# Kernel tuning notes

Measured on AMD Instinct MI355X. Metric: run time of the kernel, lower is better.

## Reference

```python
import jax, jax.numpy as jnp
import numpy as np


def setup_inputs() -> dict:
    key = jax.random.key(0)
    ks = jax.random.split(key, 6)
    B, N, D_in, D, Dg, H = 32, 256, 512, 256, 256, 512
    s = lambda f_in: 1.0 / np.sqrt(f_in)
    return {
        "xi": jax.random.normal(ks[0], (B, N, D_in), dtype=jnp.float32),
        "W_img": jax.random.normal(ks[1], (D_in, D), dtype=jnp.float32) * s(D_in),
        "b_img": jnp.zeros((D,), jnp.float32),
        "W_gnn_self": jax.random.normal(ks[2], (D, Dg), dtype=jnp.float32) * s(D),
        "W_gnn_nbr": jax.random.normal(ks[3], (D, Dg), dtype=jnp.float32) * s(D),
        "b_gnn": jnp.zeros((Dg,), jnp.float32),
        "W1": jax.random.normal(ks[4], (N * Dg, H), dtype=jnp.float32) * s(N * Dg),
        "b1": jnp.zeros((H,), jnp.float32),
        "W2": jax.random.normal(ks[5], (H, 1), dtype=jnp.float32) * s(H),
        "b2": jnp.zeros((1,), jnp.float32),
        "k": 10,
    }


def _knn_edges(xie, k):
    # xie: [B, N, D]. Per-image squared euclidean cdist + top-k (exclude self).
    B, N, _ = xie.shape
    x2 = jnp.sum(xie * xie, axis=-1)  # [B, N]
    d2 = x2[:, :, None] + x2[:, None, :] - 2.0 * jnp.einsum("bnd,bmd->bnm", xie, xie)
    big = jnp.asarray(1e30, d2.dtype)
    d2 = d2 + big * jnp.eye(N, dtype=d2.dtype)  # exclude self
    _, nbr = jax.lax.top_k(-d2, k)  # [B, N, k] neighbor (source) indices
    tgt = jnp.broadcast_to(jnp.arange(N)[None, :, None], (B, N, k))
    return nbr, tgt


def reference(xi, W_img, b_img, W_gnn_self, W_gnn_nbr, b_gnn, W1, b1, W2, b2, k):
    B, N, _ = xi.shape
    # image encoder -> per-node embeddings [B, N, D]
    xie = xi @ W_img + b_img
    # KNN graph build per image, then shift indices into one batched graph
    nbr, tgt = _knn_edges(xie, k)
    shift = (jnp.arange(B) * N)[:, None, None]
    src = (nbr + shift).reshape(-1)  # [B*N*k]
    dst = (tgt + shift).reshape(-1)  # [B*N*k]
    # batched graph conv: mean neighbor aggregation + self transform
    x_flat = xie.reshape(B * N, -1)
    agg = jax.ops.segment_sum(x_flat[src], dst, num_segments=B * N) / k
    gep = jax.nn.relu(x_flat @ W_gnn_self + agg @ W_gnn_nbr + b_gnn)
    gep = gep.reshape(B, N, -1)  # split_batch_graph
    # estimation MLP on flattened graph embedding
    h = jax.nn.relu(gep.reshape(B, -1) @ W1 + b1)
    out = h @ W2 + b2  # [B, 1]
    return xie, gep, out
```

## Files before the change

### kernel.cpp

```cpp
#include <hip/hip_runtime.h>

#define BB 32
#define NN 256
#define DIN 512
#define DD 256
#define HH 512
#define MM 8192
#define KSTR 16

typedef __attribute__((ext_vector_type(8))) __bf16 bf16x8;
typedef __attribute__((ext_vector_type(4))) float f32x4;
typedef unsigned short ushort_t;

typedef const float __attribute__((address_space(1)))* gas1f;
typedef const unsigned int __attribute__((address_space(1)))* gas1u;
typedef unsigned int __attribute__((address_space(3)))* las3u;

__device__ __forceinline__ unsigned short f2bf(float x) {
  unsigned u = __float_as_uint(x);
  u += 0x7FFFu + ((u >> 16) & 1u);
  return (unsigned short)(u >> 16);
}

__global__ __launch_bounds__(512) void k_enc(const float* __restrict__ A,
                                             const float* __restrict__ W,
                                             const float* __restrict__ bias,
                                             float* __restrict__ C,
                                             ushort_t* __restrict__ A_bf,
                                             float* __restrict__ xieT) {
  __shared__ float Asm[32][520];
  const int tid = threadIdx.x;
  const int mb0 = blockIdx.x * 32;
  const int cg = tid & 31;
  const int mh = (tid >> 5) & 7;
  const int team = tid >> 8;
#pragma unroll
  for (int i = 0; i < 8; ++i) {
    int idx = tid + i * 512;
    int m = idx >> 7;
    int kq = idx & 127;
    float4 v = *reinterpret_cast<const float4*>(&A[(size_t)(mb0 + m) * DIN + kq * 4]);
    *reinterpret_cast<float4*>(&Asm[m][kq * 4]) = v;
  }
  __syncthreads();
  float4 acc[4][2] = {};
  const int kt0 = team * 256;
  const float* wp = &W[(size_t)kt0 * DD + cg * 8];
  float4 wA[4][2], wB[4][2];
#pragma unroll
  for (int j = 0; j < 4; ++j) {
    wA[j][0] = *reinterpret_cast<const float4*>(&wp[(size_t)j * DD]);
    wA[j][1] = *reinterpret_cast<const float4*>(&wp[(size_t)j * DD + 4]);
  }
  for (int it = 0; it < 64; ++it) {
    if (it < 63) {
#pragma unroll
      for (int j = 0; j < 4; ++j) {
        wB[j][0] = *reinterpret_cast<const float4*>(&wp[(size_t)((it + 1) * 4 + j) * DD]);
        wB[j][1] = *reinterpret_cast<const float4*>(&wp[(size_t)((it + 1) * 4 + j) * DD + 4]);
      }
    }
    const int kk = kt0 + it * 4;
#pragma unroll
    for (int r = 0; r < 4; ++r) {
      float4 a = *reinterpret_cast<const float4*>(&Asm[mh * 4 + r][kk]);
#pragma unroll
      for (int h = 0; h < 2; ++h) {
        acc[r][h].x += a.x * wA[0][h].x; acc[r][h].y += a.x * wA[0][h].y;
        acc[r][h].z += a.x * wA[0][h].z; acc[r][h].w += a.x * wA[0][h].w;
        acc[r][h].x += a.y * wA[1][h].x; acc[r][h].y += a.y * wA[1][h].y;
        acc[r][h].z += a.y * wA[1][h].z; acc[r][h].w += a.y * wA[1][h].w;
        acc[r][h].x += a.z * wA[2][h].x; acc[r][h].y += a.z * wA[2][h].y;
        acc[r][h].z += a.z * wA[2][h].z; acc[r][h].w += a.z * wA[2][h].w;
        acc[r][h].x += a.w * wA[3][h].x; acc[r][h].y += a.w * wA[3][h].y;
        acc[r][h].z += a.w * wA[3][h].z; acc[r][h].w += a.w * wA[3][h].w;
      }
    }
#pragma unroll
    for (int j = 0; j < 4; ++j) {
      wA[j][0] = wB[j][0]; wA[j][1] = wB[j][1];
    }
  }
  __syncthreads();
  float* red = &Asm[0][0];
  if (team == 1) {
#pragma unroll
    for (int r = 0; r < 4; ++r) {
      *reinterpret_cast<float4*>(&red[(mh * 4 + r) * 256 + cg * 8]) = acc[r][0];
      *reinterpret_cast<float4*>(&red[(mh * 4 + r) * 256 + cg * 8 + 4]) = acc[r][1];
    }
  }
  __syncthreads();
  if (team == 0) {
    float4 bv0 = *reinterpret_cast<const float4*>(&bias[cg * 8]);
    float4 bv1 = *reinterpret_cast<const float4*>(&bias[cg * 8 + 4]);
#pragma unroll
    for (int r = 0; r < 4; ++r) {
      const int row = mb0 + mh * 4 + r;
      float4 o0 = *reinterpret_cast<float4*>(&red[(mh * 4 + r) * 256 + cg * 8]);
      float4 o1 = *reinterpret_cast<float4*>(&red[(mh * 4 + r) * 256 + cg * 8 + 4]);
      float4 s0, s1;
      s0.x = acc[r][0].x + o0.x + bv0.x; s0.y = acc[r][0].y + o0.y + bv0.y;
      s0.z = acc[r][0].z + o0.z + bv0.z; s0.w = acc[r][0].w + o0.w + bv0.w;
      s1.x = acc[r][1].x + o1.x + bv1.x; s1.y = acc[r][1].y + o1.y + bv1.y;
      s1.z = acc[r][1].z + o1.z + bv1.z; s1.w = acc[r][1].w + o1.w + bv1.w;
      *reinterpret_cast<float4*>(&C[(size_t)row * DD + cg * 8]) = s0;
      *reinterpret_cast<float4*>(&C[(size_t)row * DD + cg * 8 + 4]) = s1;
      ushort4 ob0, ob1;
      ob0.x = f2bf(s0.x); ob0.y = f2bf(s0.y); ob0.z = f2bf(s0.z); ob0.w = f2bf(s0.w);
      ob1.x = f2bf(s1.x); ob1.y = f2bf(s1.y); ob1.z = f2bf(s1.z); ob1.w = f2bf(s1.w);
      *reinterpret_cast<ushort4*>(&A_bf[(size_t)row * 512 + cg * 8]) = ob0;
      *reinterpret_cast<ushort4*>(&A_bf[(size_t)row * 512 + cg * 8 + 4]) = ob1;
      *reinterpret_cast<float4*>(&red[(mh * 4 + r) * 256 + cg * 8]) = s0;
      *reinterpret_cast<float4*>(&red[(mh * 4 + r) * 256 + cg * 8 + 4]) = s1;
    }
  }
  __syncthreads();
  {
    const int b = mb0 >> 8;
    const int n0b = mb0 & 255;
    const int d = tid >> 1;
    const int nh = (tid & 1) * 16;
    float tmp[16];
#pragma unroll
    for (int i = 0; i < 16; ++i) tmp[i] = red[(nh + i) * 256 + d];
    float* dst = &xieT[((size_t)b * 256 + d) * 256 + n0b + nh];
#pragma unroll
    for (int i = 0; i < 4; ++i)
      *reinterpret_cast<float4*>(&dst[i * 4]) = *reinterpret_cast<float4*>(&tmp[i * 4]);
  }
}

__global__ __launch_bounds__(256) void k_norm(const float* __restrict__ X,
                                              float* __restrict__ x2) {
  const int tid = threadIdx.x;
  const int row = blockIdx.x * 4 + (tid >> 6);
  const int lane = tid & 63;
  float4 v = *reinterpret_cast<const float4*>(&X[(size_t)row * DD + lane * 4]);
  float s = v.x * v.x + v.y * v.y + v.z * v.z + v.w * v.w;
#pragma unroll
  for (int off = 1; off < 64; off <<= 1) s += __shfl_xor(s, off);
  if (lane == 0) x2[row] = s;
}

__global__ __launch_bounds__(512) void k_dist(const float* __restrict__ xie,
                                              const float* __restrict__ xieT,
                                              const float* __restrict__ x2g,
                                              float* __restrict__ d2) {
  __shared__ float Asm[32][260];
  const int tid = threadIdx.x;
  const int b = blockIdx.x >> 3;
  const int n0b = (blockIdx.x & 7) * 32;
  const int base = b * 256;
  const int cg = tid & 31;
  const int rg = tid >> 5;
#pragma unroll
  for (int i = 0; i < 4; ++i) {
    int idx = tid + i * 512;
    int m = idx >> 6;
    int kq = idx & 63;
    float4 v = *reinterpret_cast<const float4*>(
        &xie[(size_t)(base + n0b + m) * DD + kq * 4]);
    *reinterpret_cast<float4*>(&Asm[m][kq * 4]) = v;
  }
  __syncthreads();
  float4 acc[2][2] = {};
  const float* wp = &xieT[(size_t)base * 256 + cg * 8];
  float4 wA[4][2], wB[4][2];
#pragma unroll
  for (int j = 0; j < 4; ++j) {
    wA[j][0] = *reinterpret_cast<const float4*>(&wp[(size_t)j * 256]);
    wA[j][1] = *reinterpret_cast<const float4*>(&wp[(size_t)j * 256 + 4]);
  }
  for (int it = 0; it < 64; ++it) {
    if (it < 63) {
#pragma unroll
      for (int j = 0; j < 4; ++j) {
        wB[j][0] = *reinterpret_cast<const float4*>(&wp[(size_t)((it + 1) * 4 + j) * 256]);
        wB[j][1] = *reinterpret_cast<const float4*>(&wp[(size_t)((it + 1) * 4 + j) * 256 + 4]);
      }
    }
#pragma unroll
    for (int r = 0; r < 2; ++r) {
      float4 a = *reinterpret_cast<const float4*>(&Asm[rg * 2 + r][it * 4]);
#pragma unroll
      for (int h = 0; h < 2; ++h) {
        acc[r][h].x += a.x * wA[0][h].x; acc[r][h].y += a.x * wA[0][h].y;
        acc[r][h].z += a.x * wA[0][h].z; acc[r][h].w += a.x * wA[0][h].w;
        acc[r][h].x += a.y * wA[1][h].x; acc[r][h].y += a.y * wA[1][h].y;
        acc[r][h].z += a.y * wA[1][h].z; acc[r][h].w += a.y * wA[1][h].w;
        acc[r][h].x += a.z * wA[2][h].x; acc[r][h].y += a.z * wA[2][h].y;
        acc[r][h].z += a.z * wA[2][h].z; acc[r][h].w += a.z * wA[2][h].w;
        acc[r][h].x += a.w * wA[3][h].x; acc[r][h].y += a.w * wA[3][h].y;
        acc[r][h].z += a.w * wA[3][h].z; acc[r][h].w += a.w * wA[3][h].w;
      }
    }
#pragma unroll
    for (int j = 0; j < 4; ++j) {
      wA[j][0] = wB[j][0]; wA[j][1] = wB[j][1];
    }
  }
#pragma unroll
  for (int r = 0; r < 2; ++r) {
    const int nl = n0b + rg * 2 + r;
    const float xn = x2g[base + nl];
#pragma unroll
    for (int h = 0; h < 2; ++h) {
      const float* accp = reinterpret_cast<const float*>(&acc[r][h]);
      float4 v;
      float* vv = reinterpret_cast<float*>(&v);
#pragma unroll
      for (int j2 = 0; j2 < 4; ++j2) {
        const int mc = cg * 8 + h * 4 + j2;
        float dv = xn + x2g[base + mc] - 2.0f * accp[j2];
        if (nl == mc) dv = 1e30f;
        vv[j2] = dv;
      }
      *reinterpret_cast<float4*>(&d2[(size_t)(base + nl) * 256 + cg * 8 + h * 4]) = v;
    }
  }
}

__global__ __launch_bounds__(256) void k_topkagg(const float* __restrict__ X,
                                                 const float* __restrict__ d2,
                                                 const int* __restrict__ kp,
                                                 ushort_t* __restrict__ A_bf) {
  __shared__ int nbrL[4][KSTR];
  const int tid = threadIdx.x;
  const int rw = tid >> 6;
  const int i = blockIdx.x * 4 + rw;
  const int lane = tid & 63;
  const int kcnt = kp[0];
  const float* row = d2 + (size_t)i * NN;
  float v0 = row[lane];
  float v1 = row[lane + 64];
  float v2 = row[lane + 128];
  float v3 = row[lane + 192];
  for (int it = 0; it < kcnt; ++it) {
    float v = v0; int idx = lane;
    if (v1 < v) { v = v1; idx = lane + 64; }
    if (v2 < v) { v = v2; idx = lane + 128; }
    if (v3 < v) { v = v3; idx = lane + 192; }
#pragma unroll
    for (int off = 1; off < 64; off <<= 1) {
      float ov = __shfl_xor(v, off);
      int oi = __shfl_xor(idx, off);
      if (ov < v || (ov == v && oi < idx)) { v = ov; idx = oi; }
    }
    if (lane == 0) nbrL[rw][it] = idx;
    const int slot = idx >> 6;
    if (lane == (idx & 63)) {
      if (slot == 0) v0 = 3e38f;
      else if (slot == 1) v1 = 3e38f;
      else if (slot == 2) v2 = 3e38f;
      else v3 = 3e38f;
    }
  }
  __syncthreads();
  {
    const int b = i >> 8;
    float4 s = make_float4(0.f, 0.f, 0.f, 0.f);
    for (int j = 0; j < kcnt; ++j) {
      const int nb = nbrL[rw][j];
      float4 v = *reinterpret_cast<const float4*>(
          &X[(size_t)(b * NN + nb) * DD + lane * 4]);
      s.x += v.x; s.y += v.y; s.z += v.z; s.w += v.w;
    }
    const float sc = 1.0f / (float)kcnt;
    ushort4 ob;
    ob.x = f2bf(s.x * sc); ob.y = f2bf(s.y * sc);
    ob.z = f2bf(s.z * sc); ob.w = f2bf(s.w * sc);
    *reinterpret_cast<ushort4*>(&A_bf[(size_t)i * 512 + 256 + lane * 4]) = ob;
  }
}

__global__ __launch_bounds__(256) void k_cvtw(const float* __restrict__ Ws,
                                              const float* __restrict__ Wn,
                                              ushort_t* __restrict__ B_bfT) {
  const int id = blockIdx.x * 256 + threadIdx.x;
  const int k = id >> 8;
  const int n = id & 255;
  float v = (k < 256) ? Ws[(size_t)k * 256 + n] : Wn[(size_t)(k - 256) * 256 + n];
  B_bfT[(size_t)n * 512 + k] = f2bf(v);
}

__global__ __launch_bounds__(256) void k_gnn(const ushort_t* __restrict__ A_bf,
                                             const ushort_t* __restrict__ B_bfT,
                                             const float* __restrict__ bias,
                                             float* __restrict__ C,
                                             ushort_t* __restrict__ gep_bf) {
  __shared__ ushort_t As[128 * 64];
  __shared__ ushort_t Bs[64 * 64];
  const int tid = threadIdx.x;
  const int m0 = blockIdx.x * 128, n0 = blockIdx.y * 64;
  const int l = tid & 63, w = tid >> 6;
  const int mw = (w & 1) * 64, nw = (w >> 1) * 32;
  f32x4 acc[4][2] = {};
  for (int kt = 0; kt < 8; ++kt) {
    const int kb = kt * 64;
    const int grow = w * 8 + (l >> 3);
    const int gcol = (l & 7) * 8;
#pragma unroll
    for (int it2 = 0; it2 < 4; ++it2) {
      __builtin_amdgcn_global_load_lds(
          (gas1u)&A_bf[(size_t)(m0 + it2 * 32 + grow) * 512 + kb + gcol],
          (las3u)((char*)As + it2 * 4096 + w * 1024), 16, 0, 0);
    }
#pragma unroll
    for (int it2 = 0; it2 < 2; ++it2) {
      __builtin_amdgcn_global_load_lds(
          (gas1u)&B_bfT[(size_t)(n0 + it2 * 32 + grow) * 512 + kb + gcol],
          (las3u)((char*)Bs + it2 * 4096 + w * 1024), 16, 0, 0);
    }
    __syncthreads();
#pragma unroll
    for (int ks = 0; ks < 2; ++ks) {
      const int koff = ks * 32 + (l >> 4) * 8;
      bf16x8 a[4], bv[2];
#pragma unroll
      for (int mi = 0; mi < 4; ++mi)
        a[mi] = *reinterpret_cast<const bf16x8*>(&As[(mw + mi * 16 + (l & 15)) * 64 + koff]);
#pragma unroll
      for (int ni = 0; ni < 2; ++ni)
        bv[ni] = *reinterpret_cast<const bf16x8*>(&Bs[(nw + ni * 16 + (l & 15)) * 64 + koff]);
#pragma unroll
      for (int mi = 0; mi < 4; ++mi)
#pragma unroll
        for (int ni = 0; ni < 2; ++ni)
          acc[mi][ni] = __builtin_amdgcn_mfma_f32_16x16x32_bf16(a[mi], bv[ni],
                                                                acc[mi][ni], 0, 0, 0);
    }
    __syncthreads();
  }
#pragma unroll
  for (int mi = 0; mi < 4; ++mi) {
    const int rb = m0 + mw + mi * 16 + (l >> 4) * 4;
#pragma unroll
    for (int ni = 0; ni < 2; ++ni) {
      const int col = n0 + nw + ni * 16 + (l & 15);
      const float bv = bias[col];
#pragma unroll
      for (int r = 0; r < 4; ++r) {
        float v = acc[mi][ni][r] + bv;
        v = v > 0.0f ? v : 0.0f;
        C[(size_t)(rb + r) * 256 + col] = v;
        gep_bf[(size_t)(rb + r) * 256 + col] = f2bf(v);
      }
    }
  }
}

__global__ __launch_bounds__(512) void k_mlp1(const ushort_t* __restrict__ gep_bf,
                                              const float* __restrict__ W1,
                                              float* __restrict__ part) {
  __shared__ ushort_t WbT[2][512][40];
  __shared__ ushort_t Ab[32][264];
  const int tid = threadIdx.x;
  const int b = blockIdx.x;
  const int l = tid & 63, w = tid >> 6;
#pragma unroll
  for (int i = 0; i < 2; ++i) {
    int id = tid + i * 512;
    int m = id >> 5, dq8 = (id & 31) * 8;
    *reinterpret_cast<uint4*>(&Ab[m][dq8]) = *reinterpret_cast<const uint4*>(
        &gep_bf[((size_t)m * 256 + b) * 256 + dq8]);
  }
  const float* Wbase = W1 + (size_t)b * 256 * 512 + tid;
  float wreg[32];
  auto WLOAD = [&](int s) {
#pragma unroll
    for (int kk = 0; kk < 32; ++kk)
      wreg[kk] = Wbase[(size_t)(s * 32 + kk) * 512];
  };
  auto WSTORE = [&](int buf) {
#pragma unroll
    for (int q = 0; q < 4; ++q) {
      ushort_t tmp[8];
#pragma unroll
      for (int j = 0; j < 8; ++j) tmp[j] = f2bf(wreg[q * 8 + j]);
      *reinterpret_cast<uint4*>(&WbT[buf][tid][q * 8]) =
          *reinterpret_cast<const uint4*>(tmp);
    }
  };
  WLOAD(0);
  WSTORE(0);
  __syncthreads();
  const int n0w = w * 64;
  f32x4 acc[2][4] = {};
  for (int s = 0; s < 8; ++s) {
    const int cur = s & 1;
    if (s < 7) WLOAD(s + 1);
    bf16x8 a[2], bw[4];
#pragma unroll
    for (int mi = 0; mi < 2; ++mi)
      a[mi] = *reinterpret_cast<const bf16x8*>(
          &Ab[mi * 16 + (l & 15)][s * 32 + (l >> 4) * 8]);
#pragma unroll
    for (int nf = 0; nf < 4; ++nf)
      bw[nf] = *reinterpret_cast<const bf16x8*>(
          &WbT[cur][n0w + nf * 16 + (l & 15)][(l >> 4) * 8]);
#pragma unroll
    for (int mi = 0; mi < 2; ++mi)
#pragma unroll
      for (int nf = 0; nf < 4; ++nf)
        acc[mi][nf] = __builtin_amdgcn_mfma_f32_16x16x32_bf16(a[mi], bw[nf],
                                                              acc[mi][nf], 0, 0, 0);
    if (s < 7) {
      WSTORE(cur ^ 1);
      __syncthreads();
    }
  }
#pragma unroll
  for (int mi = 0; mi < 2; ++mi)
#pragma unroll
    for (int nf = 0; nf < 4; ++nf) {
      const int col = n0w + nf * 16 + (l & 15);
#pragma unroll
      for (int r = 0; r < 4; ++r) {
        const int m = mi * 16 + (l >> 4) * 4 + r;
        part[((size_t)b * 32 + m) * HH + col] = acc[mi][nf][r];
      }
    }
}

__global__ __launch_bounds__(256) void k_fin(const float* __restrict__ part,
                                             const float* __restrict__ b1,
                                             const float* __restrict__ W2,
                                             const float* __restrict__ b2,
                                             float* __restrict__ outp) {
  __shared__ float red[4];
  const int tid = threadIdx.x;
  const int m = blockIdx.x;
  const int c0 = tid * 2;
  float s0 = 0.f, s1 = 0.f, s2 = 0.f, s3 = 0.f;
  for (int bb = 0; bb < 256; bb += 2) {
    float2 v0 = *reinterpret_cast<const float2*>(&part[((size_t)bb * 32 + m) * 512 + c0]);
    float2 v1 = *reinterpret_cast<const float2*>(&part[((size_t)(bb + 1) * 32 + m) * 512 + c0]);
    s0 += v0.x; s1 += v0.y; s2 += v1.x; s3 += v1.y;
  }
  float h0 = s0 + s2 + b1[c0];
  float h1 = s1 + s3 + b1[c0 + 1];
  h0 = h0 > 0.f ? h0 : 0.f;
  h1 = h1 > 0.f ? h1 : 0.f;
  float val = h0 * W2[c0] + h1 * W2[c0 + 1];
#pragma unroll
  for (int off = 1; off < 64; off <<= 1) val += __shfl_xor(val, off);
  const int w = tid >> 6;
  if ((tid & 63) == 0) red[w] = val;
  __syncthreads();
  if (tid == 0) outp[m] = red[0] + red[1] + red[2] + red[3] + b2[0];
}

extern "C" void kernel_launch(void* const* d_in, const int* in_sizes, int n_in,
                              void* d_out, int out_size, void* d_ws, size_t ws_size,
                              hipStream_t stream) {
  const float* xi     = (const float*)d_in[0];
  const float* W_img  = (const float*)d_in[1];
  const float* b_img  = (const float*)d_in[2];
  const float* W_self = (const float*)d_in[3];
  const float* W_nbr  = (const float*)d_in[4];
  const float* b_gnn  = (const float*)d_in[5];
  const float* W1     = (const float*)d_in[6];
  const float* b1     = (const float*)d_in[7];
  const float* W2     = (const float*)d_in[8];
  const float* b2     = (const float*)d_in[9];
  const int*   kp     = (const int*)d_in[10];

  float* xie  = (float*)d_out;
  float* gep  = xie + (size_t)MM * DD;
  float* outp = gep + (size_t)MM * DD;

  float* ws   = (float*)d_ws;
  float* x2   = ws;
  float* d2   = ws + 8192;
  float* part = d2 + (size_t)2097152;
  float* xieT = part + (size_t)4194304;
  ushort_t* A_bf   = (ushort_t*)(xieT + 2097152);
  ushort_t* B_bfT  = A_bf + (size_t)MM * 512;
  ushort_t* gep_bf = B_bfT + 131072;

  k_enc    <<<MM / 32, 512, 0, stream>>>(xi, W_img, b_img, xie, A_bf, xieT);
  k_cvtw   <<<512, 256, 0, stream>>>(W_self, W_nbr, B_bfT);
  k_norm   <<<MM / 4, 256, 0, stream>>>(xie, x2);
  k_dist   <<<256, 512, 0, stream>>>(xie, xieT, x2, d2);
  k_topkagg<<<MM / 4, 256, 0, stream>>>(xie, d2, kp, A_bf);
  k_gnn    <<<dim3(64, 4), 256, 0, stream>>>(A_bf, B_bfT, b_gnn, gep, gep_bf);
  k_mlp1   <<<256, 512, 0, stream>>>(gep_bf, W1, part);
  k_fin    <<<BB, 256, 0, stream>>>(part, b1, W2, b2, outp);
}
```

Baseline: 153.2 us.

## Fuse norm and weight conversion into neighbors, retile GNN GEMM, split final reduction

Computes squared row norms inside the encoder epilogue from shared memory and folds the GNN weight bf16 transpose into the distance kernel, removing two launches and a reread of xie. The GNN GEMM moves to 64x64 tiles with padded LDS and register-staged loads, doubling the block count. The final hidden-layer reduction over 256 partials is split into a parallel 256-block partial sum plus a small finishing kernel, adding more parallelism to a previously 32-block, bandwidth-bound step.

```diff
diff --git a/kernel.cpp b/kernel.cpp
--- a/kernel.cpp
+++ b/kernel.cpp
@@ -27,7 +27,8 @@
                                              const float* __restrict__ bias,
                                              float* __restrict__ C,
                                              ushort_t* __restrict__ A_bf,
-                                             float* __restrict__ xieT) {
+                                             float* __restrict__ xieT,
+                                             float* __restrict__ x2g) {
   __shared__ float Asm[32][520];
   const int tid = threadIdx.x;
   const int mb0 = blockIdx.x * 32;
@@ -117,6 +118,19 @@
   }
   __syncthreads();
   {
+    const int lane = tid & 63;
+    const int w8 = tid >> 6;
+#pragma unroll
+    for (int rr = 0; rr < 4; ++rr) {
+      const int row = w8 * 4 + rr;
+      float4 v = *reinterpret_cast<const float4*>(&red[row * 256 + lane * 4]);
+      float s = v.x * v.x + v.y * v.y + v.z * v.z + v.w * v.w;
+#pragma unroll
+      for (int off = 1; off < 64; off <<= 1) s += __shfl_xor(s, off);
+      if (lane == 0) x2g[mb0 + row] = s;
+    }
+  }
+  {
     const int b = mb0 >> 8;
     const int n0b = mb0 & 255;
     const int d = tid >> 1;
@@ -131,22 +145,13 @@
   }
 }
 
-__global__ __launch_bounds__(256) void k_norm(const float* __restrict__ X,
-                                              float* __restrict__ x2) {
-  const int tid = threadIdx.x;
-  const int row = blockIdx.x * 4 + (tid >> 6);
-  const int lane = tid & 63;
-  float4 v = *reinterpret_cast<const float4*>(&X[(size_t)row * DD + lane * 4]);
-  float s = v.x * v.x + v.y * v.y + v.z * v.z + v.w * v.w;
-#pragma unroll
-  for (int off = 1; off < 64; off <<= 1) s += __shfl_xor(s, off);
-  if (lane == 0) x2[row] = s;
-}
-
 __global__ __launch_bounds__(512) void k_dist(const float* __restrict__ xie,
                                               const float* __restrict__ xieT,
                                               const float* __restrict__ x2g,
-                                              float* __restrict__ d2) {
+                                              float* __restrict__ d2,
+                                              const float* __restrict__ Ws,
+                                              const float* __restrict__ Wn,
+                                              ushort_t* __restrict__ B_bfT) {
   __shared__ float Asm[32][260];
   const int tid = threadIdx.x;
   const int b = blockIdx.x >> 3;
@@ -218,6 +223,13 @@
       }
       *reinterpret_cast<float4*>(&d2[(size_t)(base + nl) * 256 + cg * 8 + h * 4]) = v;
     }
+  }
+  {
+    const int id = blockIdx.x * 512 + tid;
+    const int k = id >> 8;
+    const int n = id & 255;
+    float v = (k < 256) ? Ws[(size_t)k * 256 + n] : Wn[(size_t)(k - 256) * 256 + n];
+    B_bfT[(size_t)n * 512 + k] = f2bf(v);
   }
 }
 
@@ -274,67 +286,53 @@
   }
 }
 
-__global__ __launch_bounds__(256) void k_cvtw(const float* __restrict__ Ws,
-                                              const float* __restrict__ Wn,
-                                              ushort_t* __restrict__ B_bfT) {
-  const int id = blockIdx.x * 256 + threadIdx.x;
-  const int k = id >> 8;
-  const int n = id & 255;
-  float v = (k < 256) ? Ws[(size_t)k * 256 + n] : Wn[(size_t)(k - 256) * 256 + n];
-  B_bfT[(size_t)n * 512 + k] = f2bf(v);
-}
-
 __global__ __launch_bounds__(256) void k_gnn(const ushort_t* __restrict__ A_bf,
                                              const ushort_t* __restrict__ B_bfT,
                                              const float* __restrict__ bias,
                                              float* __restrict__ C,
                                              ushort_t* __restrict__ gep_bf) {
-  __shared__ ushort_t As[128 * 64];
-  __shared__ ushort_t Bs[64 * 64];
-  const int tid = threadIdx.x;
-  const int m0 = blockIdx.x * 128, n0 = blockIdx.y * 64;
+  __shared__ ushort_t As[64 * 72];
+  __shared__ ushort_t Bs[64 * 72];
+  const int tid = threadIdx.x;
+  const int m0 = blockIdx.x * 64, n0 = blockIdx.y * 64;
   const int l = tid & 63, w = tid >> 6;
-  const int mw = (w & 1) * 64, nw = (w >> 1) * 32;
-  f32x4 acc[4][2] = {};
+  const int mw = (w & 1) * 32, nw = (w >> 1) * 32;
+  const int lr = tid >> 3, lq = tid & 7;
+  f32x4 acc[2][2] = {};
   for (int kt = 0; kt < 8; ++kt) {
     const int kb = kt * 64;
-    const int grow = w * 8 + (l >> 3);
-    const int gcol = (l & 7) * 8;
-#pragma unroll
-    for (int it2 = 0; it2 < 4; ++it2) {
-      __builtin_amdgcn_global_load_lds(
-          (gas1u)&A_bf[(size_t)(m0 + it2 * 32 + grow) * 512 + kb + gcol],
-          (las3u)((char*)As + it2 * 4096 + w * 1024), 16, 0, 0);
-    }
-#pragma unroll
-    for (int it2 = 0; it2 < 2; ++it2) {
-      __builtin_amdgcn_global_load_lds(
-          (gas1u)&B_bfT[(size_t)(n0 + it2 * 32 + grow) * 512 + kb + gcol],
-          (las3u)((char*)Bs + it2 * 4096 + w * 1024), 16, 0, 0);
+#pragma unroll
+    for (int s = 0; s < 2; ++s) {
+      const int r = lr + s * 32;
+      uint4 va = *reinterpret_cast<const uint4*>(&A_bf[(size_t)(m0 + r) * 512 + kb + lq * 8]);
+      *reinterpret_cast<uint4*>(&As[r * 72 + lq * 8]) = va;
+      uint4 vb = *reinterpret_cast<const uint4*>(&B_bfT[(size_t)(n0 + r) * 512 + kb + lq * 8]);
+      *reinterpret_cast<uint4*>(&Bs[r * 72 + lq * 8]) = vb;
     }
     __syncthreads();
 #pragma unroll
     for (int ks = 0; ks < 2; ++ks) {
-      const int koff = ks * 32 + (l >> 4) * 8;
-      bf16x8 a[4], bv[2];
-#pragma unroll
-      for (int mi = 0; mi < 4; ++mi)
-        a[mi] = *reinterpret_cast<const bf16x8*>(&As[(mw + mi * 16 + (l & 15)) * 64 + koff]);
+      bf16x8 af[2], bf[2];
+#pragma unroll
+      for (int mi = 0; mi < 2; ++mi)
+        af[mi] = *reinterpret_cast<const bf16x8*>(
+            &As[(mw + mi * 16 + (l & 15)) * 72 + ks * 32 + (l >> 4) * 8]);
 #pragma unroll
       for (int ni = 0; ni < 2; ++ni)
-        bv[ni] = *reinterpret_cast<const bf16x8*>(&Bs[(nw + ni * 16 + (l & 15)) * 64 + koff]);
-#pragma unroll
-      for (int mi = 0; mi < 4; ++mi)
+        bf[ni] = *reinterpret_cast<const bf16x8*>(
+            &Bs[(nw + ni * 16 + (l & 15)) * 72 + ks * 32 + (l >> 4) * 8]);
+#pragma unroll
+      for (int mi = 0; mi < 2; ++mi)
 #pragma unroll
         for (int ni = 0; ni < 2; ++ni)
-          acc[mi][ni] = __builtin_amdgcn_mfma_f32_16x16x32_bf16(a[mi], bv[ni],
+          acc[mi][ni] = __builtin_amdgcn_mfma_f32_16x16x32_bf16(af[mi], bf[ni],
                                                                 acc[mi][ni], 0, 0, 0);
     }
     __syncthreads();
   }
 #pragma unroll
-  for (int mi = 0; mi < 4; ++mi) {
-    const int rb = m0 + mw + mi * 16 + (l >> 4) * 4;
+  for (int mi = 0; mi < 2; ++mi) {
+    const int row_base = m0 + mw + mi * 16 + (l >> 4) * 4;
 #pragma unroll
     for (int ni = 0; ni < 2; ++ni) {
       const int col = n0 + nw + ni * 16 + (l & 15);
@@ -343,8 +341,8 @@
       for (int r = 0; r < 4; ++r) {
         float v = acc[mi][ni][r] + bv;
         v = v > 0.0f ? v : 0.0f;
-        C[(size_t)(rb + r) * 256 + col] = v;
-        gep_bf[(size_t)(rb + r) * 256 + col] = f2bf(v);
+        C[(size_t)(row_base + r) * 256 + col] = v;
+        gep_bf[(size_t)(row_base + r) * 256 + col] = f2bf(v);
       }
     }
   }
@@ -423,23 +421,38 @@
     }
 }
 
-__global__ __launch_bounds__(256) void k_fin(const float* __restrict__ part,
-                                             const float* __restrict__ b1,
-                                             const float* __restrict__ W2,
-                                             const float* __restrict__ b2,
-                                             float* __restrict__ outp) {
+__global__ __launch_bounds__(256) void k_hred(const float* __restrict__ part,
+                                              float* __restrict__ hpart) {
+  const int tid = threadIdx.x;
+  const int m = blockIdx.x >> 3;
+  const int s = blockIdx.x & 7;
+  const int c0 = tid * 2;
+  float a0 = 0.f, a1 = 0.f;
+  for (int bb = s * 32; bb < s * 32 + 32; ++bb) {
+    float2 v = *reinterpret_cast<const float2*>(&part[((size_t)bb * 32 + m) * 512 + c0]);
+    a0 += v.x; a1 += v.y;
+  }
+  float2 o; o.x = a0; o.y = a1;
+  *reinterpret_cast<float2*>(&hpart[((size_t)s * 32 + m) * 512 + c0]) = o;
+}
+
+__global__ __launch_bounds__(256) void k_out2(const float* __restrict__ hpart,
+                                              const float* __restrict__ b1,
+                                              const float* __restrict__ W2,
+                                              const float* __restrict__ b2,
+                                              float* __restrict__ outp) {
   __shared__ float red[4];
   const int tid = threadIdx.x;
   const int m = blockIdx.x;
   const int c0 = tid * 2;
-  float s0 = 0.f, s1 = 0.f, s2 = 0.f, s3 = 0.f;
-  for (int bb = 0; bb < 256; bb += 2) {
-    float2 v0 = *reinterpret_cast<const float2*>(&part[((size_t)bb * 32 + m) * 512 + c0]);
-    float2 v1 = *reinterpret_cast<const float2*>(&part[((size_t)(bb + 1) * 32 + m) * 512 + c0]);
-    s0 += v0.x; s1 += v0.y; s2 += v1.x; s3 += v1.y;
-  }
-  float h0 = s0 + s2 + b1[c0];
-  float h1 = s1 + s3 + b1[c0 + 1];
+  float a0 = 0.f, a1 = 0.f;
+#pragma unroll
+  for (int s = 0; s < 8; ++s) {
+    float2 v = *reinterpret_cast<const float2*>(&hpart[((size_t)s * 32 + m) * 512 + c0]);
+    a0 += v.x; a1 += v.y;
+  }
+  float h0 = a0 + b1[c0];
+  float h1 = a1 + b1[c0 + 1];
   h0 = h0 > 0.f ? h0 : 0.f;
   h1 = h1 > 0.f ? h1 : 0.f;
   float val = h0 * W2[c0] + h1 * W2[c0 + 1];
@@ -475,16 +488,16 @@
   float* d2   = ws + 8192;
   float* part = d2 + (size_t)2097152;
   float* xieT = part + (size_t)4194304;
-  ushort_t* A_bf   = (ushort_t*)(xieT + 2097152);
+  float* hpart = xieT + (size_t)2097152;
+  ushort_t* A_bf   = (ushort_t*)(hpart + 131072);
   ushort_t* B_bfT  = A_bf + (size_t)MM * 512;
   ushort_t* gep_bf = B_bfT + 131072;
 
-  k_enc    <<<MM / 32, 512, 0, stream>>>(xi, W_img, b_img, xie, A_bf, xieT);
-  k_cvtw   <<<512, 256, 0, stream>>>(W_self, W_nbr, B_bfT);
-  k_norm   <<<MM / 4, 256, 0, stream>>>(xie, x2);
-  k_dist   <<<256, 512, 0, stream>>>(xie, xieT, x2, d2);
+  k_enc    <<<MM / 32, 512, 0, stream>>>(xi, W_img, b_img, xie, A_bf, xieT, x2);
+  k_dist   <<<256, 512, 0, stream>>>(xie, xieT, x2, d2, W_self, W_nbr, B_bfT);
   k_topkagg<<<MM / 4, 256, 0, stream>>>(xie, d2, kp, A_bf);
-  k_gnn    <<<dim3(64, 4), 256, 0, stream>>>(A_bf, B_bfT, b_gnn, gep, gep_bf);
+  k_gnn    <<<dim3(128, 4), 256, 0, stream>>>(A_bf, B_bfT, b_gnn, gep, gep_bf);
   k_mlp1   <<<256, 512, 0, stream>>>(gep_bf, W1, part);
-  k_fin    <<<BB, 256, 0, stream>>>(part, b1, W2, b2, outp);
-}
+  k_hred   <<<256, 256, 0, stream>>>(part, hpart);
+  k_out2   <<<BB, 256, 0, stream>>>(hpart, b1, W2, b2, outp);
+}
```

Measured after the change: 136.2 us. -11.1%, faster.
